# Kernel tuning notes

Hardware: AMD Instinct MI355X
Metric: run time of the kernel (lower is better)

The kernel has to match this reference:

```python
import jax, jax.numpy as jnp
import numpy as np

N_EVENTS = 4_000_000
HW = 128          # DVS sensor resolution
TICKS = 10_000    # simulation horizon
KH, KW = 3, 3     # kernel_size
OUT_CH = 64       # out_channels


def setup_inputs() -> dict:
    key = jax.random.key(0)
    k1, k2, k3 = jax.random.split(key, 3)
    return {
        "values": jnp.ones((N_EVENTS,), dtype=jnp.float32),            # spike value 1.0 per add_spike
        "ticks_in": jax.random.randint(k1, (N_EVENTS,), 0, TICKS, dtype=jnp.int32),
        "xs": jax.random.randint(k2, (N_EVENTS,), 0, HW, dtype=jnp.int32),
        "ys": jax.random.randint(k3, (N_EVENTS,), 0, HW, dtype=jnp.int32),
        "stride": 1,
    }


def reference(values, ticks_in, xs, ys, stride):
    """Event-driven spike routing of Conv2dT.forward.

    Returns the per-channel synapse input buffers [OUT_CH, KH*KW, TICKS]:
    buffer[c, s, t] = total spike value scattered into synapse s of soma c at tick t.
    (The subsequent izh-soma ODE simulation lives in the external ABM model.)
    """
    S = KH * KW
    off_y = jnp.repeat(jnp.arange(KH), KW)   # [S], ky per synapse_idx = ky*KW + kx
    off_x = jnp.tile(jnp.arange(KW), KH)     # [S], kx per synapse_idx

    out_x = xs[None, :] - off_x[:, None]     # [S, N]
    out_y = ys[None, :] - off_y[:, None]     # [S, N]
    valid = (out_x >= 0) & (out_y >= 0) & (out_x % stride == 0) & (out_y % stride == 0)
    contrib = jnp.where(valid, values[None, :], jnp.zeros((), values.dtype))  # [S, N]

    # scatter-add over ticks for each synapse offset
    buf = jnp.zeros((S, TICKS), dtype=values.dtype)
    buf = buf.at[jnp.arange(S)[:, None], ticks_in[None, :]].add(contrib)     # [S, T]

    # every output channel receives the identical spike dispatch
    return jnp.broadcast_to(buf[None], (OUT_CH, S, TICKS))
```

## Files before the change

### kernel.cpp

```cpp
#include <hip/hip_runtime.h>

#define TICKS 10000
#define NSYN 9
#define OUT_CH 64

#define SCATTER_BLOCKS 256
#define SCATTER_THREADS 1024

__global__ void zero_kernel(float* __restrict__ p, int n) {
    int i = blockIdx.x * blockDim.x + threadIdx.x;
    if (i < n) p[i] = 0.0f;
}

__global__ __launch_bounds__(SCATTER_THREADS) void scatter_kernel(
    const float* __restrict__ values,
    const int*   __restrict__ ticks,
    const int*   __restrict__ xs,
    const int*   __restrict__ ys,
    const int*   __restrict__ stride_p,
    float*       __restrict__ hist,
    int n)
{
    __shared__ float lhist[TICKS];
    const int stride = stride_p[0];
    const int tid = threadIdx.x;

    if (stride == 1) {
        for (int j = tid; j < TICKS; j += SCATTER_THREADS) lhist[j] = 0.0f;
        __syncthreads();

        const int n4  = n >> 2;
        const int gsz = gridDim.x * SCATTER_THREADS;
        const float4* __restrict__ v4 = (const float4*)values;
        const int4*   __restrict__ t4 = (const int4*)ticks;
        const int4*   __restrict__ x4 = (const int4*)xs;
        const int4*   __restrict__ y4 = (const int4*)ys;

        for (int i = blockIdx.x * SCATTER_THREADS + tid; i < n4; i += gsz) {
            float4 v = v4[i];
            int4   t = t4[i];
            int4   x = x4[i];
            int4   y = y4[i];

            if (x.x >= 2 && y.x >= 2) atomicAdd(&lhist[t.x], v.x);
            else atomicAdd(&hist[(min(y.x, 2) * 3 + min(x.x, 2)) * TICKS + t.x], v.x);

            if (x.y >= 2 && y.y >= 2) atomicAdd(&lhist[t.y], v.y);
            else atomicAdd(&hist[(min(y.y, 2) * 3 + min(x.y, 2)) * TICKS + t.y], v.y);

            if (x.z >= 2 && y.z >= 2) atomicAdd(&lhist[t.z], v.z);
            else atomicAdd(&hist[(min(y.z, 2) * 3 + min(x.z, 2)) * TICKS + t.z], v.z);

            if (x.w >= 2 && y.w >= 2) atomicAdd(&lhist[t.w], v.w);
            else atomicAdd(&hist[(min(y.w, 2) * 3 + min(x.w, 2)) * TICKS + t.w], v.w);
        }

        if (blockIdx.x == 0 && tid == 0) {
            for (int i = n4 << 2; i < n; ++i) {
                atomicAdd(&hist[(min(ys[i], 2) * 3 + min(xs[i], 2)) * TICKS + ticks[i]],
                          values[i]);
            }
        }

        __syncthreads();

        int phase = (blockIdx.x * 157) % TICKS;
        for (int j = tid; j < TICKS; j += SCATTER_THREADS) {
            int b = j + phase;
            if (b >= TICKS) b -= TICKS;
            float v = lhist[b];
            if (v != 0.0f) atomicAdd(&hist[8 * TICKS + b], v);
        }
    } else {
        const int gsz = gridDim.x * SCATTER_THREADS;
        for (int i = blockIdx.x * SCATTER_THREADS + tid; i < n; i += gsz) {
            float v = values[i];
            int   t = ticks[i];
            int   x = xs[i];
            int   y = ys[i];
            #pragma unroll
            for (int ky = 0; ky < 3; ++ky) {
                int oy = y - ky;
                if (oy < 0 || (oy % stride) != 0) continue;
                #pragma unroll
                for (int kx = 0; kx < 3; ++kx) {
                    int ox = x - kx;
                    if (ox < 0 || (ox % stride) != 0) continue;
                    atomicAdd(&hist[(ky * 3 + kx) * TICKS + t], v);
                }
            }
        }
    }
}

__global__ __launch_bounds__(256) void emit_kernel(
    const float* __restrict__ hist,
    const int*   __restrict__ stride_p,
    float*       __restrict__ out)
{
    int t = blockIdx.x * blockDim.x + threadIdx.x;
    if (t >= TICKS) return;
    const int stride = stride_p[0];

    float b[NSYN];
    #pragma unroll
    for (int s = 0; s < NSYN; ++s) b[s] = hist[s * TICKS + t];

    if (stride == 1) {
        #pragma unroll
        for (int r = 0; r < 3; ++r) {
            b[r * 3 + 1] += b[r * 3 + 2];
            b[r * 3 + 0] += b[r * 3 + 1];
        }
        #pragma unroll
        for (int c = 0; c < 3; ++c) {
            b[3 + c] += b[6 + c];
            b[0 + c] += b[3 + c];
        }
    }

    for (int c = blockIdx.y; c < OUT_CH; c += gridDim.y) {
        #pragma unroll
        for (int s = 0; s < NSYN; ++s) {
            out[(c * NSYN + s) * TICKS + t] = b[s];
        }
    }
}

extern "C" void kernel_launch(void* const* d_in, const int* in_sizes, int n_in,
                              void* d_out, int out_size, void* d_ws, size_t ws_size,
                              hipStream_t stream) {
    const float* values   = (const float*)d_in[0];
    const int*   ticks    = (const int*)  d_in[1];
    const int*   xs       = (const int*)  d_in[2];
    const int*   ys       = (const int*)  d_in[3];
    const int*   stride_p = (const int*)  d_in[4];
    float*       out      = (float*)      d_out;
    const int n = in_sizes[0];

    const size_t hist_bytes = (size_t)NSYN * TICKS * sizeof(float);
    float* hist;
    bool hist_in_out;
    if (ws_size >= hist_bytes) {
        hist = (float*)d_ws;
        hist_in_out = false;
    } else {
        hist = out;
        hist_in_out = true;
    }

    {
        int nh = NSYN * TICKS;
        zero_kernel<<<(nh + 255) / 256, 256, 0, stream>>>(hist, nh);
    }

    scatter_kernel<<<SCATTER_BLOCKS, SCATTER_THREADS, 0, stream>>>(
        values, ticks, xs, ys, stride_p, hist, n);

    {
        dim3 grid((TICKS + 255) / 256, hist_in_out ? 1 : 64);
        emit_kernel<<<grid, 256, 0, stream>>>(hist, stride_p, out);
    }
}
```

Before: 134.9 us.

## Flush per-block LDS histograms to workspace and reduce in a separate kernel

```diff
diff --git a/kernel.cpp b/kernel.cpp
--- a/kernel.cpp
+++ b/kernel.cpp
@@ -6,6 +6,8 @@
 
 #define SCATTER_BLOCKS 256
 #define SCATTER_THREADS 1024
+#define RED_SEG 8
+#define RED_Y (SCATTER_BLOCKS / RED_SEG)
 
 __global__ void zero_kernel(float* __restrict__ p, int n) {
     int i = blockIdx.x * blockDim.x + threadIdx.x;
@@ -19,9 +21,10 @@
     const int*   __restrict__ ys,
     const int*   __restrict__ stride_p,
     float*       __restrict__ hist,
+    float*       __restrict__ partial,
     int n)
 {
-    __shared__ float lhist[TICKS];
+    __shared__ __align__(16) float lhist[TICKS];
     const int stride = stride_p[0];
     const int tid = threadIdx.x;
 
@@ -64,12 +67,19 @@
 
         __syncthreads();
 
-        int phase = (blockIdx.x * 157) % TICKS;
-        for (int j = tid; j < TICKS; j += SCATTER_THREADS) {
-            int b = j + phase;
-            if (b >= TICKS) b -= TICKS;
-            float v = lhist[b];
-            if (v != 0.0f) atomicAdd(&hist[8 * TICKS + b], v);
+        if (partial != nullptr) {
+            float4* __restrict__ dst =
+                (float4*)(partial + (size_t)blockIdx.x * TICKS);
+            const float4* __restrict__ src = (const float4*)lhist;
+            for (int j = tid; j < TICKS / 4; j += SCATTER_THREADS) dst[j] = src[j];
+        } else {
+            int phase = (blockIdx.x * 157) % TICKS;
+            for (int j = tid; j < TICKS; j += SCATTER_THREADS) {
+                int b = j + phase;
+                if (b >= TICKS) b -= TICKS;
+                float v = lhist[b];
+                if (v != 0.0f) atomicAdd(&hist[8 * TICKS + b], v);
+            }
         }
     } else {
         const int gsz = gridDim.x * SCATTER_THREADS;
@@ -93,6 +103,30 @@
     }
 }
 
+__global__ __launch_bounds__(256) void reduce_kernel(
+    const float* __restrict__ partial,
+    const int*   __restrict__ stride_p,
+    float*       __restrict__ hist)
+{
+    if (stride_p[0] != 1) return;
+    int c = blockIdx.x * 256 + threadIdx.x;
+    if (c >= TICKS / 4) return;
+
+    const float4* __restrict__ p4 = (const float4*)partial;
+    const int base = blockIdx.y * RED_SEG;
+    float ax = 0.f, ay = 0.f, az = 0.f, aw = 0.f;
+    #pragma unroll
+    for (int k = 0; k < RED_SEG; ++k) {
+        float4 v = p4[(size_t)(base + k) * (TICKS / 4) + c];
+        ax += v.x; ay += v.y; az += v.z; aw += v.w;
+    }
+    float* h = hist + 8 * TICKS + c * 4;
+    atomicAdd(h + 0, ax);
+    atomicAdd(h + 1, ay);
+    atomicAdd(h + 2, az);
+    atomicAdd(h + 3, aw);
+}
+
 __global__ __launch_bounds__(256) void emit_kernel(
     const float* __restrict__ hist,
     const int*   __restrict__ stride_p,
@@ -122,7 +156,7 @@
     for (int c = blockIdx.y; c < OUT_CH; c += gridDim.y) {
         #pragma unroll
         for (int s = 0; s < NSYN; ++s) {
-            out[(c * NSYN + s) * TICKS + t] = b[s];
+            __builtin_nontemporal_store(b[s], &out[(c * NSYN + s) * TICKS + t]);
         }
     }
 }
@@ -139,9 +173,16 @@
     const int n = in_sizes[0];
 
     const size_t hist_bytes = (size_t)NSYN * TICKS * sizeof(float);
+    const size_t part_bytes = (size_t)SCATTER_BLOCKS * TICKS * sizeof(float);
+
     float* hist;
+    float* partial = nullptr;
     bool hist_in_out;
-    if (ws_size >= hist_bytes) {
+    if (ws_size >= hist_bytes + part_bytes) {
+        hist = (float*)d_ws;
+        partial = (float*)d_ws + (size_t)NSYN * TICKS;
+        hist_in_out = false;
+    } else if (ws_size >= hist_bytes) {
         hist = (float*)d_ws;
         hist_in_out = false;
     } else {
@@ -155,7 +196,12 @@
     }
 
     scatter_kernel<<<SCATTER_BLOCKS, SCATTER_THREADS, 0, stream>>>(
-        values, ticks, xs, ys, stride_p, hist, n);
+        values, ticks, xs, ys, stride_p, hist, partial, n);
+
+    if (partial != nullptr) {
+        dim3 rg((TICKS / 4 + 255) / 256, RED_Y);
+        reduce_kernel<<<rg, 256, 0, stream>>>(partial, stride_p, hist);
+    }
 
     {
         dim3 grid((TICKS + 255) / 256, hist_in_out ? 1 : 64);
```

After: 133.6 us. Within noise of the previous version (-1.0%).
